# Kernel tuning notes

Hardware: AMD Instinct MI355X
Metric: run time of the kernel (lower is better)

Reference implementation:

```python
import jax, jax.numpy as jnp
import numpy as np

B, N, H, NH = 2, 2048, 256, 8
D = H // NH           # head dim = 32
SPATIAL = NH * 7      # 3 points + 1 distance + 3 direction per head
LN_EPS = 1e-5


def layer_norm(x, g, b):
    m = jnp.mean(x, axis=-1, keepdims=True)
    v = jnp.mean(jnp.square(x - m), axis=-1, keepdims=True)
    return (x - m) * jax.lax.rsqrt(v + LN_EPS) * g + b


def setup_inputs() -> dict:
    key = jax.random.key(0)
    ks = jax.random.split(key, 12)
    s = 0.02
    return {
        "x": jax.random.normal(ks[0], (B, N, H), jnp.float32),
        "pos_CA": jax.random.normal(ks[1], (B, N, 3), jnp.float32),
        "pos_CB": jax.random.normal(ks[2], (B, N, 3), jnp.float32),
        "frame": jax.random.normal(ks[3], (B, N, 3, 3), jnp.float32),
        "mask": jnp.ones((B, N), dtype=bool),
        # linear weights stored [in, out] so y = x @ W + b
        "Wq": jax.random.normal(ks[4], (H, H), jnp.float32) * s,
        "bq": jnp.zeros((H,), jnp.float32),
        "Wk": jax.random.normal(ks[5], (H, H), jnp.float32) * s,
        "bk": jnp.zeros((H,), jnp.float32),
        "Wv": jax.random.normal(ks[6], (H, H), jnp.float32) * s,
        "bv": jnp.zeros((H,), jnp.float32),
        "W_out": jax.random.normal(ks[7], (H + SPATIAL, H), jnp.float32) * s,
        "b_out": jnp.zeros((H,), jnp.float32),
        "ln1_g": jnp.ones((H,), jnp.float32),
        "ln1_b": jnp.zeros((H,), jnp.float32),
        "ln2_g": jnp.ones((H,), jnp.float32),
        "ln2_b": jnp.zeros((H,), jnp.float32),
    }


def reference(x, pos_CA, pos_CB, frame, mask, Wq, bq, Wk, bk, Wv, bv,
              W_out, b_out, ln1_g, ln1_b, ln2_g, ln2_b):
    b, n, hdim = x.shape
    q = (x @ Wq + bq).reshape(b, n, NH, D)
    k = (x @ Wk + bk).reshape(b, n, NH, D)
    v = (x @ Wv + bv).reshape(b, n, NH, D)

    # logits [b, l, k, h] (note: no 1/sqrt(d) scaling in the original)
    logits = jnp.einsum('blhd,bkhd->blkh', q, k)
    m2 = (mask[:, :, None] & mask[:, None, :])[..., None]  # [b,l,k,1]
    logits = jnp.where(m2, logits, -jnp.inf)
    alpha = jax.nn.softmax(logits, axis=2)  # softmax over k

    feat_node = jnp.einsum('blkh,bkhd->blhd', alpha, v).reshape(b, n, hdim)

    # rel_pos[b,l,k] = CB[l] - CA[k]
    rel_pos = pos_CB[:, :, None, :] - pos_CA[:, None, :, :]  # [b,l,k,3]
    atom_pos_bias = jnp.einsum('blkh,blkd->blhd', alpha, rel_pos)  # [b,l,h,3]

    feat_distance = jnp.linalg.norm(atom_pos_bias, axis=-1, keepdims=True)  # [b,l,h,1]
    feat_points = jnp.einsum('blij,blhj->blhi', frame, atom_pos_bias)       # [b,l,h,3]
    feat_direction = feat_points / (
        jnp.linalg.norm(feat_points, axis=-1, keepdims=True) + 1e-10)

    feat_spatial = jnp.concatenate([
        feat_points.reshape(b, n, NH * 3),
        feat_distance.reshape(b, n, NH),
        feat_direction.reshape(b, n, NH * 3),
    ], axis=-1)

    feat_all = jnp.concatenate([feat_node, feat_spatial], axis=-1)
    y = jax.nn.relu(feat_all @ W_out + b_out)
    y = layer_norm(y, ln1_g, ln1_b)
    y = jnp.where(mask[..., None], y, 0.0)
    # hidden dims match -> residual path
    return layer_norm(x + y, ln2_g, ln2_b)
```

## Files before the change

kernel.cpp:

```cpp
#include <hip/hip_runtime.h>
#include <math.h>

#define B_ 2
#define N_ 2048
#define H_ 256
#define NH_ 8
#define D_ 32
#define FEAT_ 312
#define FEATP_ 320

typedef __attribute__((ext_vector_type(8))) short bf16x8;
typedef __attribute__((ext_vector_type(4))) short s16x4;
typedef __attribute__((ext_vector_type(4))) float f32x4;

__device__ __forceinline__ short f2bf(float f) {
    unsigned int u = __float_as_uint(f);
    unsigned int r = (u + 0x7fffu + ((u >> 16) & 1u)) >> 16;
    return (short)(unsigned short)r;
}

__global__ __launch_bounds__(256) void prep_kernel(
    const float* __restrict__ x, const float* __restrict__ Wq,
    const float* __restrict__ Wk, const float* __restrict__ Wv,
    const float* __restrict__ Wout, const float* __restrict__ pos_CA,
    short* __restrict__ xb, short* __restrict__ Wt, short* __restrict__ Wot,
    short* __restrict__ caT, short* __restrict__ featb)
{
    const int t = blockIdx.x * 256 + threadIdx.x;
    for (int i = t; i < (B_ * N_ * H_) / 4; i += 65536) {
        float4 v = *(const float4*)(x + (size_t)i * 4);
        s16x4 o;
        o[0] = f2bf(v.x); o[1] = f2bf(v.y); o[2] = f2bf(v.z); o[3] = f2bf(v.w);
        *(s16x4*)(xb + (size_t)i * 4) = o;
    }
    for (int i = t; i < 768 * 256; i += 65536) {
        int n = i >> 8, kk = i & 255;
        int region = n >> 8, nn = n & 255;
        const float* W = region == 0 ? Wq : (region == 1 ? Wk : Wv);
        Wt[i] = f2bf(W[kk * 256 + nn]);
    }
    for (int i = t; i < 256 * FEATP_; i += 65536) {
        int n = i / FEATP_, kk = i % FEATP_;
        Wot[i] = f2bf(kk < FEAT_ ? Wout[kk * 256 + n] : 0.f);
    }
    if (t < 6 * N_) {
        int d6 = t >> 11, n = t & (N_ - 1);
        int bb = d6 / 3, dd = d6 % 3;
        caT[t] = f2bf(pos_CA[((size_t)bb * N_ + n) * 3 + dd]);
    }
    if (t < B_ * N_ * 8) {
        int l = t >> 3, c = FEAT_ + (t & 7);
        featb[(size_t)l * FEATP_ + c] = 0;
    }
}

__global__ __launch_bounds__(256) void qkv_gemm(
    const short* __restrict__ xb, const short* __restrict__ Wt,
    const float* __restrict__ bq, const float* __restrict__ bk,
    const float* __restrict__ bv,
    short* __restrict__ qb, short* __restrict__ kb, short* __restrict__ vT)
{
    const int wave = threadIdx.x >> 6, lane = threadIdx.x & 63;
    const int quad = lane >> 4, col = lane & 15;
    const int n0 = blockIdx.x * 128 + (wave & 1) * 64;
    const int m0 = blockIdx.y * 64 + (wave >> 1) * 32;

    f32x4 acc[2][4];
#pragma unroll
    for (int i = 0; i < 2; ++i)
#pragma unroll
        for (int j = 0; j < 4; ++j) acc[i][j] = (f32x4){0.f, 0.f, 0.f, 0.f};

#pragma unroll
    for (int k0 = 0; k0 < 256; k0 += 32) {
        bf16x8 af[2], bfr[4];
#pragma unroll
        for (int i = 0; i < 2; ++i)
            af[i] = *(const bf16x8*)(xb + (size_t)(m0 + i * 16 + col) * 256 + k0 + quad * 8);
#pragma unroll
        for (int j = 0; j < 4; ++j)
            bfr[j] = *(const bf16x8*)(Wt + (size_t)(n0 + j * 16 + col) * 256 + k0 + quad * 8);
#pragma unroll
        for (int i = 0; i < 2; ++i)
#pragma unroll
            for (int j = 0; j < 4; ++j)
                acc[i][j] = __builtin_amdgcn_mfma_f32_16x16x32_bf16(af[i], bfr[j], acc[i][j], 0, 0, 0);
    }

    const int region = blockIdx.x >> 1;
    const float* bias = region == 0 ? bq : (region == 1 ? bk : bv);
    float bo[4];
#pragma unroll
    for (int j = 0; j < 4; ++j) bo[j] = bias[(n0 + j * 16 + col) & 255];

    if (region < 2) {
        short* dst = region == 0 ? qb : kb;
#pragma unroll
        for (int i = 0; i < 2; ++i)
#pragma unroll
            for (int j = 0; j < 4; ++j)
#pragma unroll
                for (int r = 0; r < 4; ++r)
                    dst[(size_t)(m0 + i * 16 + quad * 4 + r) * 256 +
                        ((n0 + j * 16 + col) & 255)] = f2bf(acc[i][j][r] + bo[j]);
    } else {
#pragma unroll
        for (int i = 0; i < 2; ++i) {
            const int gl0 = m0 + i * 16 + quad * 4;
            const int bb = gl0 >> 11, l0 = gl0 & (N_ - 1);
#pragma unroll
            for (int j = 0; j < 4; ++j) {
                const int vcol = (n0 + j * 16 + col) & 255;
                const int hh = vcol >> 5, dd = vcol & 31;
                s16x4 pk;
#pragma unroll
                for (int r = 0; r < 4; ++r) pk[r] = f2bf(acc[i][j][r] + bo[j]);
                *(s16x4*)(vT + (size_t)((bb * 8 + hh) * 32 + dd) * N_ + l0) = pk;
            }
        }
    }
}

__global__ __launch_bounds__(512) void attn_kernel(
    const short* __restrict__ qg, const short* __restrict__ kgb,
    const short* __restrict__ vTg, const short* __restrict__ caT,
    const float* __restrict__ pos_CB, const float* __restrict__ frame,
    short* __restrict__ featb)
{
    const int bx = blockIdx.x;
    const int lt = bx & 31, h = (bx >> 5) & 7, b = bx >> 8;
    const int tid = threadIdx.x;
    const int wave = tid >> 6, lane = tid & 63;
    const int kg = wave >> 2, wl = wave & 3;
    const int quad = lane >> 4, col = lane & 15;

    __shared__ short Ks[2][64 * 40];
    __shared__ short VT[2][48 * 72];
    __shared__ short Pw[8][16 * 72];
    __shared__ float Obuf[4][16][40];

    for (int i = tid; i < 2 * 13 * 72; i += 512) {
        int g = i / (13 * 72), r = i % (13 * 72);
        VT[g][35 * 72 + r] = 0;
    }

    const int l_base = lt * 64 + wl * 16;
    const bf16x8 qfrag =
        *(const bf16x8*)(qg + ((size_t)(b * N_ + l_base + col)) * H_ + h * D_ + quad * 8);

    f32x4 accO[3];
#pragma unroll
    for (int dt = 0; dt < 3; ++dt) accO[dt] = (f32x4){0.f, 0.f, 0.f, 0.f};
    float srun = 0.f;

    const short* kbase = kgb + (size_t)(b * N_) * H_ + h * D_;
    const short* vTb = vTg + (size_t)((b * 8 + h) * 32) * N_;
    const short* caTb = caT + (size_t)(b * 3) * N_;

    const int local = tid & 255;
    const int krow = local >> 2, seg = local & 3;
    const int vd = local >> 3, vseg = local & 7;
    const int kofs = kg * 1024;

    for (int it = 0; it < 16; ++it) {
        const int k0 = kofs + it * 64;
        __syncthreads();
        *(float4*)&Ks[kg][krow * 40 + seg * 8] =
            *(const float4*)(kbase + (size_t)(k0 + krow) * H_ + seg * 8);
        *(float4*)&VT[kg][vd * 72 + vseg * 8] =
            *(const float4*)(vTb + (size_t)vd * N_ + k0 + vseg * 8);
        if (local < 192) {
            int d = local >> 6, kr = local & 63;
            VT[kg][(32 + d) * 72 + kr] = caTb[(size_t)d * N_ + k0 + kr];
        }
        __syncthreads();

        float p16[16];
#pragma unroll
        for (int t = 0; t < 4; ++t) {
            const bf16x8 kfrag = *(const bf16x8*)&Ks[kg][(t * 16 + col) * 40 + quad * 8];
            f32x4 z4 = (f32x4){0.f, 0.f, 0.f, 0.f};
            f32x4 s = __builtin_amdgcn_mfma_f32_16x16x32_bf16(kfrag, qfrag, z4, 0, 0, 0);
#pragma unroll
            for (int r = 0; r < 4; ++r) {
                float e = __expf(s[r]);
                srun += e;
                p16[t * 4 + r] = e;
            }
        }
#pragma unroll
        for (int t = 0; t < 4; ++t) {
            s16x4 pk;
#pragma unroll
            for (int r = 0; r < 4; ++r) pk[r] = f2bf(p16[t * 4 + r]);
            *(s16x4*)&Pw[wave][col * 72 + t * 16 + quad * 4] = pk;
        }
#pragma unroll
        for (int half = 0; half < 2; ++half) {
            const bf16x8 pfrag =
                *(const bf16x8*)&Pw[wave][col * 72 + half * 32 + quad * 8];
#pragma unroll
            for (int dt = 0; dt < 3; ++dt) {
                const bf16x8 vfrag =
                    *(const bf16x8*)&VT[kg][(dt * 16 + col) * 72 + half * 32 + quad * 8];
                accO[dt] = __builtin_amdgcn_mfma_f32_16x16x32_bf16(pfrag, vfrag, accO[dt], 0, 0, 0);
            }
        }
    }

    srun += __shfl_xor(srun, 16);
    srun += __shfl_xor(srun, 32);

    if (kg == 1) {
#pragma unroll
        for (int dt = 0; dt < 2; ++dt)
#pragma unroll
            for (int r = 0; r < 4; ++r)
                Obuf[wl][quad * 4 + r][dt * 16 + col] = accO[dt][r];
        if (col < 3)
#pragma unroll
            for (int r = 0; r < 4; ++r)
                Obuf[wl][quad * 4 + r][32 + col] = accO[2][r];
        if (quad == 0) Obuf[wl][col][35] = srun;
    }
    __syncthreads();
    if (kg == 0) {
        if (quad == 0) Obuf[wl][col][35] += srun;
        float inv[4];
#pragma unroll
        for (int r = 0; r < 4; ++r) inv[r] = 1.f / Obuf[wl][quad * 4 + r][35];

#pragma unroll
        for (int dt = 0; dt < 2; ++dt)
#pragma unroll
            for (int r = 0; r < 4; ++r) {
                float o = (accO[dt][r] + Obuf[wl][quad * 4 + r][dt * 16 + col]) * inv[r];
                featb[(size_t)(b * N_ + l_base + quad * 4 + r) * FEATP_ +
                      h * D_ + dt * 16 + col] = f2bf(o);
            }
        if (col < 3)
#pragma unroll
            for (int r = 0; r < 4; ++r)
                Obuf[wl][quad * 4 + r][36 + col] =
                    (accO[2][r] + Obuf[wl][quad * 4 + r][32 + col]) * inv[r];

        if (lane < 16) {
            const int l = l_base + lane;
            const float ox = Obuf[wl][lane][36];
            const float oy = Obuf[wl][lane][37];
            const float oz = Obuf[wl][lane][38];
            const float* pcb = pos_CB + (size_t)(b * N_ + l) * 3;
            const float ax = pcb[0] - ox, ay = pcb[1] - oy, az = pcb[2] - oz;
            const float* fr = frame + (size_t)(b * N_ + l) * 9;
            const float p0 = fr[0] * ax + fr[1] * ay + fr[2] * az;
            const float p1 = fr[3] * ax + fr[4] * ay + fr[5] * az;
            const float p2 = fr[6] * ax + fr[7] * ay + fr[8] * az;
            const float dist = sqrtf(ax * ax + ay * ay + az * az);
            const float pn = sqrtf(p0 * p0 + p1 * p1 + p2 * p2);
            const float rinv = 1.f / (pn + 1e-10f);
            short* fb = featb + (size_t)(b * N_ + l) * FEATP_;
            fb[256 + h * 3 + 0] = f2bf(p0);
            fb[256 + h * 3 + 1] = f2bf(p1);
            fb[256 + h * 3 + 2] = f2bf(p2);
            fb[280 + h] = f2bf(dist);
            fb[288 + h * 3 + 0] = f2bf(p0 * rinv);
            fb[288 + h * 3 + 1] = f2bf(p1 * rinv);
            fb[288 + h * 3 + 2] = f2bf(p2 * rinv);
        }
    }
}

__global__ __launch_bounds__(256) void out_gemm(
    const short* __restrict__ featb, const short* __restrict__ Wot,
    const float* __restrict__ bout, float* __restrict__ y)
{
    const int wave = threadIdx.x >> 6, lane = threadIdx.x & 63;
    const int quad = lane >> 4, col = lane & 15;
    const int n0 = blockIdx.x * 64 + (wave & 1) * 32;
    const int m0 = blockIdx.y * 32 + (wave >> 1) * 16;

    f32x4 acc[2];
    acc[0] = (f32x4){0.f, 0.f, 0.f, 0.f};
    acc[1] = (f32x4){0.f, 0.f, 0.f, 0.f};

#pragma unroll
    for (int k0 = 0; k0 < FEATP_; k0 += 32) {
        const bf16x8 af = *(const bf16x8*)(featb + (size_t)(m0 + col) * FEATP_ + k0 + quad * 8);
#pragma unroll
        for (int j = 0; j < 2; ++j) {
            const bf16x8 bfr =
                *(const bf16x8*)(Wot + (size_t)(n0 + j * 16 + col) * FEATP_ + k0 + quad * 8);
            acc[j] = __builtin_amdgcn_mfma_f32_16x16x32_bf16(af, bfr, acc[j], 0, 0, 0);
        }
    }
    float bo[2];
#pragma unroll
    for (int j = 0; j < 2; ++j) bo[j] = bout[n0 + j * 16 + col];
#pragma unroll
    for (int j = 0; j < 2; ++j)
#pragma unroll
        for (int r = 0; r < 4; ++r)
            y[(size_t)(m0 + quad * 4 + r) * 256 + n0 + j * 16 + col] =
                fmaxf(acc[j][r] + bo[j], 0.f);
}

__global__ __launch_bounds__(256) void ln_kernel(
    const float* __restrict__ y, const float* __restrict__ x,
    const float* __restrict__ g1, const float* __restrict__ b1,
    const float* __restrict__ g2, const float* __restrict__ b2,
    float* __restrict__ out)
{
    const int wave = threadIdx.x >> 6, lane = threadIdx.x & 63;
    const int row = blockIdx.x * 4 + wave;
    const size_t base = (size_t)row * 256 + lane * 4;
    float4 yv = *(const float4*)(y + base);
    float s = yv.x + yv.y + yv.z + yv.w;
    float q2 = yv.x * yv.x + yv.y * yv.y + yv.z * yv.z + yv.w * yv.w;
#pragma unroll
    for (int off = 32; off >= 1; off >>= 1) {
        s += __shfl_xor(s, off);
        q2 += __shfl_xor(q2, off);
    }
    float mean = s * (1.f / 256.f);
    float var = q2 * (1.f / 256.f) - mean * mean;
    float rs = rsqrtf(var + 1e-5f);
    const float4 g1v = *(const float4*)(g1 + lane * 4);
    const float4 b1v = *(const float4*)(b1 + lane * 4);
    const float4 xv = *(const float4*)(x + base);
    float4 z;
    z.x = xv.x + (yv.x - mean) * rs * g1v.x + b1v.x;
    z.y = xv.y + (yv.y - mean) * rs * g1v.y + b1v.y;
    z.z = xv.z + (yv.z - mean) * rs * g1v.z + b1v.z;
    z.w = xv.w + (yv.w - mean) * rs * g1v.w + b1v.w;
    float s2 = z.x + z.y + z.z + z.w;
    float qq = z.x * z.x + z.y * z.y + z.z * z.z + z.w * z.w;
#pragma unroll
    for (int off = 32; off >= 1; off >>= 1) {
        s2 += __shfl_xor(s2, off);
        qq += __shfl_xor(qq, off);
    }
    float mean2 = s2 * (1.f / 256.f);
    float var2 = qq * (1.f / 256.f) - mean2 * mean2;
    float rs2 = rsqrtf(var2 + 1e-5f);
    const float4 g2v = *(const float4*)(g2 + lane * 4);
    const float4 b2v = *(const float4*)(b2 + lane * 4);
    float4 o;
    o.x = (z.x - mean2) * rs2 * g2v.x + b2v.x;
    o.y = (z.y - mean2) * rs2 * g2v.y + b2v.y;
    o.z = (z.z - mean2) * rs2 * g2v.z + b2v.z;
    o.w = (z.w - mean2) * rs2 * g2v.w + b2v.w;
    *(float4*)(out + base) = o;
}

extern "C" void kernel_launch(void* const* d_in, const int* in_sizes, int n_in,
                              void* d_out, int out_size, void* d_ws, size_t ws_size,
                              hipStream_t stream) {
    const float* x      = (const float*)d_in[0];
    const float* pos_CA = (const float*)d_in[1];
    const float* pos_CB = (const float*)d_in[2];
    const float* frame  = (const float*)d_in[3];
    const float* Wq   = (const float*)d_in[5];
    const float* bq   = (const float*)d_in[6];
    const float* Wk   = (const float*)d_in[7];
    const float* bk   = (const float*)d_in[8];
    const float* Wv   = (const float*)d_in[9];
    const float* bv   = (const float*)d_in[10];
    const float* Wout = (const float*)d_in[11];
    const float* bout = (const float*)d_in[12];
    const float* g1   = (const float*)d_in[13];
    const float* b1   = (const float*)d_in[14];
    const float* g2   = (const float*)d_in[15];
    const float* b2   = (const float*)d_in[16];

    char* ws = (char*)d_ws;
    short* xb    = (short*)(ws);
    short* qb    = (short*)(ws + (2u << 20));
    short* kb    = (short*)(ws + (4u << 20));
    short* vT    = (short*)(ws + (6u << 20));
    short* Wt    = (short*)(ws + (8u << 20));
    short* Wot   = (short*)(ws + (8u << 20) + 393216);
    short* caT   = (short*)(ws + (8u << 20) + 557056);
    short* featb = (short*)(ws + (9u << 20));
    float* yb    = (float*)(ws + (12u << 20));

    prep_kernel<<<256, 256, 0, stream>>>(x, Wq, Wk, Wv, Wout, pos_CA,
                                         xb, Wt, Wot, caT, featb);
    qkv_gemm<<<dim3(6, 64), 256, 0, stream>>>(xb, Wt, bq, bk, bv, qb, kb, vT);
    attn_kernel<<<512, 512, 0, stream>>>(qb, kb, vT, caT, pos_CB, frame, featb);
    out_gemm<<<dim3(4, 128), 256, 0, stream>>>(featb, Wot, bout, yb);
    ln_kernel<<<1024, 256, 0, stream>>>(yb, x, g1, b1, g2, b2, (float*)d_out);
}
```

Baseline: 145.2 us.

## Prefetch K/V tiles into registers and fuse output GEMM with layer norms

The attention loop now loads the next K, V and CA tile into registers while the current tile is being computed. This replaces the load-then-sync pattern with a single barrier at the end of each iteration, so global latency overlaps with the MFMA work. Separately, the output projection GEMM and the two layer norms are merged into one kernel: each block computes 16 full rows and reduces the row statistics through shared memory. This removes the fp32 y round-trip through global memory and one kernel launch, at the cost of fewer blocks (256) and higher register pressure.

After: 144.1 us. About the same (-0.8%).

```diff
diff --git a/kernel.cpp b/kernel.cpp
--- a/kernel.cpp
+++ b/kernel.cpp
@@ -160,20 +160,25 @@
     const int local = tid & 255;
     const int krow = local >> 2, seg = local & 3;
     const int vd = local >> 3, vseg = local & 7;
+    const int cad = local >> 6, cak = local & 63;
     const int kofs = kg * 1024;
 
+    float4 kreg = *(const float4*)(kbase + (size_t)(kofs + krow) * H_ + seg * 8);
+    float4 vreg = *(const float4*)(vTb + (size_t)vd * N_ + kofs + vseg * 8);
+    short careg = (local < 192) ? caTb[(size_t)cad * N_ + kofs + cak] : (short)0;
+
     for (int it = 0; it < 16; ++it) {
-        const int k0 = kofs + it * 64;
+        *(float4*)&Ks[kg][krow * 40 + seg * 8] = kreg;
+        *(float4*)&VT[kg][vd * 72 + vseg * 8] = vreg;
+        if (local < 192) VT[kg][(32 + cad) * 72 + cak] = careg;
         __syncthreads();
-        *(float4*)&Ks[kg][krow * 40 + seg * 8] =
-            *(const float4*)(kbase + (size_t)(k0 + krow) * H_ + seg * 8);
-        *(float4*)&VT[kg][vd * 72 + vseg * 8] =
-            *(const float4*)(vTb + (size_t)vd * N_ + k0 + vseg * 8);
-        if (local < 192) {
-            int d = local >> 6, kr = local & 63;
-            VT[kg][(32 + d) * 72 + kr] = caTb[(size_t)d * N_ + k0 + kr];
-        }
-        __syncthreads();
+
+        if (it < 15) {
+            const int k0 = kofs + (it + 1) * 64;
+            kreg = *(const float4*)(kbase + (size_t)(k0 + krow) * H_ + seg * 8);
+            vreg = *(const float4*)(vTb + (size_t)vd * N_ + k0 + vseg * 8);
+            if (local < 192) careg = caTb[(size_t)cad * N_ + k0 + cak];
+        }
 
         float p16[16];
 #pragma unroll
@@ -206,6 +211,7 @@
                 accO[dt] = __builtin_amdgcn_mfma_f32_16x16x32_bf16(pfrag, vfrag, accO[dt], 0, 0, 0);
             }
         }
+        __syncthreads();
     }
 
     srun += __shfl_xor(srun, 16);
@@ -270,86 +276,115 @@
     }
 }
 
-__global__ __launch_bounds__(256) void out_gemm(
+__global__ __launch_bounds__(256) void out_ln(
     const short* __restrict__ featb, const short* __restrict__ Wot,
-    const float* __restrict__ bout, float* __restrict__ y)
-{
-    const int wave = threadIdx.x >> 6, lane = threadIdx.x & 63;
-    const int quad = lane >> 4, col = lane & 15;
-    const int n0 = blockIdx.x * 64 + (wave & 1) * 32;
-    const int m0 = blockIdx.y * 32 + (wave >> 1) * 16;
-
-    f32x4 acc[2];
-    acc[0] = (f32x4){0.f, 0.f, 0.f, 0.f};
-    acc[1] = (f32x4){0.f, 0.f, 0.f, 0.f};
-
-#pragma unroll
-    for (int k0 = 0; k0 < FEATP_; k0 += 32) {
-        const bf16x8 af = *(const bf16x8*)(featb + (size_t)(m0 + col) * FEATP_ + k0 + quad * 8);
-#pragma unroll
-        for (int j = 0; j < 2; ++j) {
-            const bf16x8 bfr =
-                *(const bf16x8*)(Wot + (size_t)(n0 + j * 16 + col) * FEATP_ + k0 + quad * 8);
-            acc[j] = __builtin_amdgcn_mfma_f32_16x16x32_bf16(af, bfr, acc[j], 0, 0, 0);
-        }
-    }
-    float bo[2];
-#pragma unroll
-    for (int j = 0; j < 2; ++j) bo[j] = bout[n0 + j * 16 + col];
-#pragma unroll
-    for (int j = 0; j < 2; ++j)
-#pragma unroll
-        for (int r = 0; r < 4; ++r)
-            y[(size_t)(m0 + quad * 4 + r) * 256 + n0 + j * 16 + col] =
-                fmaxf(acc[j][r] + bo[j], 0.f);
-}
-
-__global__ __launch_bounds__(256) void ln_kernel(
-    const float* __restrict__ y, const float* __restrict__ x,
+    const float* __restrict__ bout, const float* __restrict__ x,
     const float* __restrict__ g1, const float* __restrict__ b1,
     const float* __restrict__ g2, const float* __restrict__ b2,
     float* __restrict__ out)
 {
     const int wave = threadIdx.x >> 6, lane = threadIdx.x & 63;
-    const int row = blockIdx.x * 4 + wave;
-    const size_t base = (size_t)row * 256 + lane * 4;
-    float4 yv = *(const float4*)(y + base);
-    float s = yv.x + yv.y + yv.z + yv.w;
-    float q2 = yv.x * yv.x + yv.y * yv.y + yv.z * yv.z + yv.w * yv.w;
-#pragma unroll
-    for (int off = 32; off >= 1; off >>= 1) {
-        s += __shfl_xor(s, off);
-        q2 += __shfl_xor(q2, off);
-    }
-    float mean = s * (1.f / 256.f);
-    float var = q2 * (1.f / 256.f) - mean * mean;
-    float rs = rsqrtf(var + 1e-5f);
-    const float4 g1v = *(const float4*)(g1 + lane * 4);
-    const float4 b1v = *(const float4*)(b1 + lane * 4);
-    const float4 xv = *(const float4*)(x + base);
-    float4 z;
-    z.x = xv.x + (yv.x - mean) * rs * g1v.x + b1v.x;
-    z.y = xv.y + (yv.y - mean) * rs * g1v.y + b1v.y;
-    z.z = xv.z + (yv.z - mean) * rs * g1v.z + b1v.z;
-    z.w = xv.w + (yv.w - mean) * rs * g1v.w + b1v.w;
-    float s2 = z.x + z.y + z.z + z.w;
-    float qq = z.x * z.x + z.y * z.y + z.z * z.z + z.w * z.w;
-#pragma unroll
-    for (int off = 32; off >= 1; off >>= 1) {
-        s2 += __shfl_xor(s2, off);
-        qq += __shfl_xor(qq, off);
-    }
-    float mean2 = s2 * (1.f / 256.f);
-    float var2 = qq * (1.f / 256.f) - mean2 * mean2;
-    float rs2 = rsqrtf(var2 + 1e-5f);
-    const float4 g2v = *(const float4*)(g2 + lane * 4);
-    const float4 b2v = *(const float4*)(b2 + lane * 4);
-    float4 o;
-    o.x = (z.x - mean2) * rs2 * g2v.x + b2v.x;
-    o.y = (z.y - mean2) * rs2 * g2v.y + b2v.y;
-    o.z = (z.z - mean2) * rs2 * g2v.z + b2v.z;
-    o.w = (z.w - mean2) * rs2 * g2v.w + b2v.w;
-    *(float4*)(out + base) = o;
+    const int quad = lane >> 4, col = lane & 15;
+    const int m0 = blockIdx.x * 16;
+    const int n0 = wave * 64;
+
+    f32x4 acc[4];
+#pragma unroll
+    for (int j = 0; j < 4; ++j) acc[j] = (f32x4){0.f, 0.f, 0.f, 0.f};
+
+#pragma unroll
+    for (int k0 = 0; k0 < FEATP_; k0 += 32) {
+        const bf16x8 af = *(const bf16x8*)(featb + (size_t)(m0 + col) * FEATP_ + k0 + quad * 8);
+#pragma unroll
+        for (int j = 0; j < 4; ++j) {
+            const bf16x8 bfr =
+                *(const bf16x8*)(Wot + (size_t)(n0 + j * 16 + col) * FEATP_ + k0 + quad * 8);
+            acc[j] = __builtin_amdgcn_mfma_f32_16x16x32_bf16(af, bfr, acc[j], 0, 0, 0);
+        }
+    }
+
+    __shared__ float red[4][16][2];
+    float yv[4][4], s[4], q2[4];
+#pragma unroll
+    for (int r = 0; r < 4; ++r) { s[r] = 0.f; q2[r] = 0.f; }
+#pragma unroll
+    for (int j = 0; j < 4; ++j) {
+        const float bo = bout[n0 + j * 16 + col];
+#pragma unroll
+        for (int r = 0; r < 4; ++r) {
+            float t = fmaxf(acc[j][r] + bo, 0.f);
+            yv[j][r] = t; s[r] += t; q2[r] += t * t;
+        }
+    }
+#pragma unroll
+    for (int off = 1; off <= 8; off <<= 1)
+#pragma unroll
+        for (int r = 0; r < 4; ++r) {
+            s[r] += __shfl_xor(s[r], off);
+            q2[r] += __shfl_xor(q2[r], off);
+        }
+    if (col == 0)
+#pragma unroll
+        for (int r = 0; r < 4; ++r) {
+            red[wave][quad * 4 + r][0] = s[r];
+            red[wave][quad * 4 + r][1] = q2[r];
+        }
+    __syncthreads();
+
+    float zv[4][4], s2[4], qq[4];
+#pragma unroll
+    for (int r = 0; r < 4; ++r) { s2[r] = 0.f; qq[r] = 0.f; }
+    float mean1[4], rs1[4];
+#pragma unroll
+    for (int r = 0; r < 4; ++r) {
+        const int row = quad * 4 + r;
+        float S = red[0][row][0] + red[1][row][0] + red[2][row][0] + red[3][row][0];
+        float Q = red[0][row][1] + red[1][row][1] + red[2][row][1] + red[3][row][1];
+        mean1[r] = S * (1.f / 256.f);
+        float var = Q * (1.f / 256.f) - mean1[r] * mean1[r];
+        rs1[r] = rsqrtf(var + 1e-5f);
+    }
+#pragma unroll
+    for (int j = 0; j < 4; ++j) {
+        const int colg = n0 + j * 16 + col;
+        const float g1v = g1[colg], b1v = b1[colg];
+#pragma unroll
+        for (int r = 0; r < 4; ++r) {
+            float yn = (yv[j][r] - mean1[r]) * rs1[r] * g1v + b1v;
+            float z = x[(size_t)(m0 + quad * 4 + r) * H_ + colg] + yn;
+            zv[j][r] = z; s2[r] += z; qq[r] += z * z;
+        }
+    }
+#pragma unroll
+    for (int off = 1; off <= 8; off <<= 1)
+#pragma unroll
+        for (int r = 0; r < 4; ++r) {
+            s2[r] += __shfl_xor(s2[r], off);
+            qq[r] += __shfl_xor(qq[r], off);
+        }
+    __syncthreads();
+    if (col == 0)
+#pragma unroll
+        for (int r = 0; r < 4; ++r) {
+            red[wave][quad * 4 + r][0] = s2[r];
+            red[wave][quad * 4 + r][1] = qq[r];
+        }
+    __syncthreads();
+#pragma unroll
+    for (int r = 0; r < 4; ++r) {
+        const int row = quad * 4 + r;
+        float S = red[0][row][0] + red[1][row][0] + red[2][row][0] + red[3][row][0];
+        float Q = red[0][row][1] + red[1][row][1] + red[2][row][1] + red[3][row][1];
+        float mean2 = S * (1.f / 256.f);
+        float var2 = Q * (1.f / 256.f) - mean2 * mean2;
+        float rs2 = rsqrtf(var2 + 1e-5f);
+#pragma unroll
+        for (int j = 0; j < 4; ++j) {
+            const int colg = n0 + j * 16 + col;
+            out[(size_t)(m0 + row) * H_ + colg] =
+                (zv[j][r] - mean2) * rs2 * g2[colg] + b2[colg];
+        }
+    }
 }
 
 extern "C" void kernel_launch(void* const* d_in, const int* in_sizes, int n_in,
@@ -381,12 +416,11 @@
     short* Wot   = (short*)(ws + (8u << 20) + 393216);
     short* caT   = (short*)(ws + (8u << 20) + 557056);
     short* featb = (short*)(ws + (9u << 20));
-    float* yb    = (float*)(ws + (12u << 20));
 
     prep_kernel<<<256, 256, 0, stream>>>(x, Wq, Wk, Wv, Wout, pos_CA,
                                          xb, Wt, Wot, caT, featb);
     qkv_gemm<<<dim3(6, 64), 256, 0, stream>>>(xb, Wt, bq, bk, bv, qb, kb, vT);
     attn_kernel<<<512, 512, 0, stream>>>(qb, kb, vT, caT, pos_CB, frame, featb);
-    out_gemm<<<dim3(4, 128), 256, 0, stream>>>(featb, Wot, bout, yb);
-    ln_kernel<<<1024, 256, 0, stream>>>(yb, x, g1, b1, g2, b2, (float*)d_out);
-}
+    out_ln<<<256, 256, 0, stream>>>(featb, Wot, bout, x, g1, b1, g2, b2,
+                                    (float*)d_out);
+}
```
